# Performance work log

Hardware: AMD Instinct MI355X
Metric: run time of the kernel (lower is better)

Reference implementation:

```python
import jax, jax.numpy as jnp
import numpy as np

EPS = 1e-8

def setup_inputs() -> dict:
    key = jax.random.key(0)
    k1, k2, k3 = jax.random.split(key, 3)
    B, A = 4, 2048
    positions = jax.random.normal(k1, (B, A, 3), dtype=jnp.float32)
    neighbors = jax.random.randint(k2, (B, A, A), 0, A, dtype=jnp.int64)
    neighbor_mask = jax.random.randint(k3, (B, A), 0, 2).astype(bool)
    return {"positions": positions, "neighbors": neighbors, "neighbor_mask": neighbor_mask}

def _safe_norm(dist_vec):
    # torch.norm has zero (sub)gradient at 0; guard sqrt for jax parity
    d2 = jnp.sum(dist_vec * dist_vec, axis=-1)  # [B, A, N]
    safe = jnp.sqrt(jnp.where(d2 > 0, d2, 1.0))
    return jnp.where(d2 > 0, safe, 0.0)

def reference(positions, neighbors, neighbor_mask):
    B, A, _ = positions.shape
    # gather neighbor positions: pos_xyz[b, i, j] = positions[b, neighbors[b, i, j]]
    pos_xyz = positions[jnp.arange(B)[:, None, None], neighbors]  # [B, A, N, 3]
    dist_vec = pos_xyz - positions[:, :, None, :]                  # [B, A, N, 3]
    distances = _safe_norm(dist_vec)                               # [B, A, N]
    distances = 1.0 / (distances + EPS)
    # pairwise mask = outer product of per-atom mask (requires N == A)
    mask2 = neighbor_mask[:, :, None] & neighbor_mask[:, None, :]  # [B, A, A]
    eye = jnp.eye(A, dtype=bool)[None]
    distances = jnp.where(eye, 0.0, distances)   # zero diagonal
    distances = jnp.where(mask2, distances, 0.0)  # mask out invalid pairs
    return distances
```

## Files before the change

### kernel.cpp

```cpp
#include <hip/hip_runtime.h>


typedef float f4 __attribute__((ext_vector_type(4)));
typedef float f2 __attribute__((ext_vector_type(2)));

constexpr int A_DIM = 2048;
constexpr int WPB   = 8;
constexpr int NTHR  = WPB * 64;

__global__ __launch_bounds__(NTHR, 8) void atom_distances_kernel(
    const float* __restrict__ pos,
    const int*   __restrict__ nbr,
    const int*   __restrict__ mask,
    float*       __restrict__ out) {
  __shared__ float    sx[A_DIM];
  __shared__ f2       syz[A_DIM];
  __shared__ unsigned smaskbits[A_DIM / 32];

  const int blocks_per_b = A_DIM / WPB;
  const int b  = blockIdx.x / blocks_per_b;
  const int i0 = (blockIdx.x % blocks_per_b) * WPB;

  const float* posb  = pos  + (size_t)b * A_DIM * 3;
  const int*   maskb = mask + (size_t)b * A_DIM;

  for (int t = threadIdx.x; t < A_DIM; t += NTHR) {
    sx[t] = posb[3 * t + 0];
    f2 yz; yz.x = posb[3 * t + 1]; yz.y = posb[3 * t + 2];
    syz[t] = yz;
  }
  for (int r = 0; r < A_DIM / NTHR; ++r) {
    const int t = r * NTHR + threadIdx.x;
    const unsigned long long bal = __ballot(maskb[t] != 0);
    if ((threadIdx.x & 63) == 0) {
      const int wbase = t >> 5;
      smaskbits[wbase]     = (unsigned)bal;
      smaskbits[wbase + 1] = (unsigned)(bal >> 32);
    }
  }
  __syncthreads();

  const int w    = threadIdx.x >> 6;
  const int lane = threadIdx.x & 63;
  const int i    = i0 + w;

  float* orow = out + ((size_t)b * A_DIM + i) * A_DIM;
  const unsigned mi = (smaskbits[i >> 5] >> (i & 31)) & 1u;

  if (mi == 0) {
    const f4 z = {0.f, 0.f, 0.f, 0.f};
    #pragma unroll
    for (int c = 0; c < 8; ++c)
      __builtin_nontemporal_store(z, reinterpret_cast<f4*>(orow + (c * 64 + lane) * 4));
    return;
  }

  const float pix  = sx[i];
  const f2    piyz = syz[i];
  const int*  nrow = nbr + ((size_t)b * A_DIM + i) * A_DIM;

#define LDN(c) (*reinterpret_cast<const int4*>(nrow + ((c) * 64 + lane) * 4))

#define ELEM(nt_, e_, dst_) { \
    const bool on_ = ((((wbits >> (bit + e_)) & 1u) != 0u) & (i != j0 + e_)); \
    const int t_ = on_ ? ((nt_) & (A_DIM - 1)) : 0; \
    const float xx_ = sx[t_]; \
    const f2 yz_ = syz[t_]; \
    const float dx_ = xx_ - pix; \
    const float dy_ = yz_.x - piyz.x; \
    const float dz_ = yz_.y - piyz.y; \
    const float d2_ = dx_ * dx_ + dy_ * dy_ + dz_ * dz_; \
    const float inv_ = d2_ > 0.0f ? __builtin_amdgcn_rsqf(d2_) : 1e8f; \
    dst_ = on_ ? inv_ : 0.0f; }

#define PROC(c, n) { \
    const int j0 = ((c) * 64 + lane) * 4; \
    const unsigned wbits = smaskbits[(c) * 8 + (lane >> 3)]; \
    const int bit = (lane & 7) * 4; \
    f4 r; \
    ELEM(n.x, 0, r.x); \
    ELEM(n.y, 1, r.y); \
    ELEM(n.z, 2, r.z); \
    ELEM(n.w, 3, r.w); \
    __builtin_nontemporal_store(r, reinterpret_cast<f4*>(orow + j0)); }

  int4 n0 = LDN(0), n1 = LDN(1), n2 = LDN(2), n3 = LDN(3);
  PROC(0, n0); n0 = LDN(4);
  PROC(1, n1); n1 = LDN(5);
  PROC(2, n2); n2 = LDN(6);
  PROC(3, n3); n3 = LDN(7);
  PROC(4, n0);
  PROC(5, n1);
  PROC(6, n2);
  PROC(7, n3);

#undef PROC
#undef ELEM
#undef LDN
}

extern "C" void kernel_launch(void* const* d_in, const int* in_sizes, int n_in,
                              void* d_out, int out_size, void* d_ws, size_t ws_size,
                              hipStream_t stream) {
  const float* pos  = (const float*)d_in[0];
  const int*   nbr  = (const int*)d_in[1];
  const int*   mask = (const int*)d_in[2];
  float*       out  = (float*)d_out;

  const int B = in_sizes[2] / A_DIM;
  const int grid = B * (A_DIM / WPB);

  atom_distances_kernel<<<grid, NTHR, 0, stream>>>(pos, nbr, mask, out);
}
```

Measured before the change: 22.35 us.

## Process two rows per wave and prefetch neighbor indices before shared-memory setup

Each block now handles 16 rows, so each wave processes two rows. This halves the number of blocks and the per-block shared-memory loading of positions and mask bits. The first neighbor-index loads are issued before the shared-memory fill and barrier, so global load latency overlaps with setup, and the rsq select becomes fminf. It adds register pressure and code size from the two-row and mixed-mask paths, and halves grid parallelism.

```diff
diff --git a/kernel.cpp b/kernel.cpp
--- a/kernel.cpp
+++ b/kernel.cpp
@@ -6,6 +6,7 @@
 
 constexpr int A_DIM = 2048;
 constexpr int WPB   = 8;
+constexpr int RPB   = 16;
 constexpr int NTHR  = WPB * 64;
 
 __global__ __launch_bounds__(NTHR, 8) void atom_distances_kernel(
@@ -17,12 +18,29 @@
   __shared__ f2       syz[A_DIM];
   __shared__ unsigned smaskbits[A_DIM / 32];
 
-  const int blocks_per_b = A_DIM / WPB;
+  const int blocks_per_b = A_DIM / RPB;
   const int b  = blockIdx.x / blocks_per_b;
-  const int i0 = (blockIdx.x % blocks_per_b) * WPB;
+  const int i0 = (blockIdx.x % blocks_per_b) * RPB;
 
   const float* posb  = pos  + (size_t)b * A_DIM * 3;
   const int*   maskb = mask + (size_t)b * A_DIM;
+
+  const int w    = threadIdx.x >> 6;
+  const int lane = threadIdx.x & 63;
+  const int iA   = i0 + w;
+  const int iB   = i0 + WPB + w;
+
+  const int miA = maskb[iA];
+  const int miB = maskb[iB];
+  const int* nrowA = nbr + ((size_t)b * A_DIM + iA) * A_DIM;
+  const int* nrowB = nbr + ((size_t)b * A_DIM + iB) * A_DIM;
+
+#define LDA(c) (*reinterpret_cast<const int4*>(nrowA + ((c) * 64 + lane) * 4))
+#define LDB(c) (*reinterpret_cast<const int4*>(nrowB + ((c) * 64 + lane) * 4))
+
+  int4 a0, a1, b0, b1;
+  if (miA) { a0 = LDA(0); a1 = LDA(1); }
+  if (miB) { b0 = LDB(0); b1 = LDB(1); }
 
   for (int t = threadIdx.x; t < A_DIM; t += NTHR) {
     sx[t] = posb[3 * t + 0];
@@ -40,63 +58,92 @@
   }
   __syncthreads();
 
-  const int w    = threadIdx.x >> 6;
-  const int lane = threadIdx.x & 63;
-  const int i    = i0 + w;
+  float* orowA = out + ((size_t)b * A_DIM + iA) * A_DIM;
+  float* orowB = out + ((size_t)b * A_DIM + iB) * A_DIM;
+  const f4 zf4 = {0.f, 0.f, 0.f, 0.f};
 
-  float* orow = out + ((size_t)b * A_DIM + i) * A_DIM;
-  const unsigned mi = (smaskbits[i >> 5] >> (i & 31)) & 1u;
+#define ZST(o_, c_) __builtin_nontemporal_store(zf4, \
+    reinterpret_cast<f4*>((o_) + ((c_) * 64 + lane) * 4))
 
-  if (mi == 0) {
-    const f4 z = {0.f, 0.f, 0.f, 0.f};
+  if (!miA && !miB) {
     #pragma unroll
-    for (int c = 0; c < 8; ++c)
-      __builtin_nontemporal_store(z, reinterpret_cast<f4*>(orow + (c * 64 + lane) * 4));
+    for (int c = 0; c < 8; ++c) { ZST(orowA, c); ZST(orowB, c); }
     return;
   }
 
-  const float pix  = sx[i];
-  const f2    piyz = syz[i];
-  const int*  nrow = nbr + ((size_t)b * A_DIM + i) * A_DIM;
-
-#define LDN(c) (*reinterpret_cast<const int4*>(nrow + ((c) * 64 + lane) * 4))
-
-#define ELEM(nt_, e_, dst_) { \
-    const bool on_ = ((((wbits >> (bit + e_)) & 1u) != 0u) & (i != j0 + e_)); \
+#define ELEM(nt_, e_, dst_, i_, pix_, piyz_) { \
+    const bool on_ = ((((wbits >> (bit + e_)) & 1u) != 0u) & ((i_) != j0 + e_)); \
     const int t_ = on_ ? ((nt_) & (A_DIM - 1)) : 0; \
     const float xx_ = sx[t_]; \
     const f2 yz_ = syz[t_]; \
-    const float dx_ = xx_ - pix; \
-    const float dy_ = yz_.x - piyz.x; \
-    const float dz_ = yz_.y - piyz.y; \
+    const float dx_ = xx_ - pix_; \
+    const float dy_ = yz_.x - piyz_.x; \
+    const float dz_ = yz_.y - piyz_.y; \
     const float d2_ = dx_ * dx_ + dy_ * dy_ + dz_ * dz_; \
-    const float inv_ = d2_ > 0.0f ? __builtin_amdgcn_rsqf(d2_) : 1e8f; \
+    const float inv_ = fminf(__builtin_amdgcn_rsqf(d2_), 1e8f); \
     dst_ = on_ ? inv_ : 0.0f; }
 
-#define PROC(c, n) { \
+#define CHUNKHDR(c) \
     const int j0 = ((c) * 64 + lane) * 4; \
     const unsigned wbits = smaskbits[(c) * 8 + (lane >> 3)]; \
-    const int bit = (lane & 7) * 4; \
-    f4 r; \
-    ELEM(n.x, 0, r.x); \
-    ELEM(n.y, 1, r.y); \
-    ELEM(n.z, 2, r.z); \
-    ELEM(n.w, 3, r.w); \
-    __builtin_nontemporal_store(r, reinterpret_cast<f4*>(orow + j0)); }
+    const int bit = (lane & 7) * 4;
 
-  int4 n0 = LDN(0), n1 = LDN(1), n2 = LDN(2), n3 = LDN(3);
-  PROC(0, n0); n0 = LDN(4);
-  PROC(1, n1); n1 = LDN(5);
-  PROC(2, n2); n2 = LDN(6);
-  PROC(3, n3); n3 = LDN(7);
-  PROC(4, n0);
-  PROC(5, n1);
-  PROC(6, n2);
-  PROC(7, n3);
+#define PROC4(n_, i_, pix_, piyz_, orow_) { \
+    f4 r_; \
+    ELEM(n_.x, 0, r_.x, i_, pix_, piyz_); \
+    ELEM(n_.y, 1, r_.y, i_, pix_, piyz_); \
+    ELEM(n_.z, 2, r_.z, i_, pix_, piyz_); \
+    ELEM(n_.w, 3, r_.w, i_, pix_, piyz_); \
+    __builtin_nontemporal_store(r_, reinterpret_cast<f4*>((orow_) + j0)); }
 
-#undef PROC
+  if (miA && miB) {
+    const float pixA = sx[iA]; const f2 piyzA = syz[iA];
+    const float pixB = sx[iB]; const f2 piyzB = syz[iB];
+    { CHUNKHDR(0); PROC4(a0, iA, pixA, piyzA, orowA); PROC4(b0, iB, pixB, piyzB, orowB); }
+    a0 = LDA(2); b0 = LDB(2);
+    { CHUNKHDR(1); PROC4(a1, iA, pixA, piyzA, orowA); PROC4(b1, iB, pixB, piyzB, orowB); }
+    a1 = LDA(3); b1 = LDB(3);
+    { CHUNKHDR(2); PROC4(a0, iA, pixA, piyzA, orowA); PROC4(b0, iB, pixB, piyzB, orowB); }
+    a0 = LDA(4); b0 = LDB(4);
+    { CHUNKHDR(3); PROC4(a1, iA, pixA, piyzA, orowA); PROC4(b1, iB, pixB, piyzB, orowB); }
+    a1 = LDA(5); b1 = LDB(5);
+    { CHUNKHDR(4); PROC4(a0, iA, pixA, piyzA, orowA); PROC4(b0, iB, pixB, piyzB, orowB); }
+    a0 = LDA(6); b0 = LDB(6);
+    { CHUNKHDR(5); PROC4(a1, iA, pixA, piyzA, orowA); PROC4(b1, iB, pixB, piyzB, orowB); }
+    a1 = LDA(7); b1 = LDB(7);
+    { CHUNKHDR(6); PROC4(a0, iA, pixA, piyzA, orowA); PROC4(b0, iB, pixB, piyzB, orowB); }
+    { CHUNKHDR(7); PROC4(a1, iA, pixA, piyzA, orowA); PROC4(b1, iB, pixB, piyzB, orowB); }
+    return;
+  }
+
+  const int    i1    = miA ? iA : iB;
+  const int*   nrow1 = miA ? nrowA : nrowB;
+  float*       orow1 = miA ? orowA : orowB;
+  float*       orow0 = miA ? orowB : orowA;
+  int4 n0 = miA ? a0 : b0;
+  int4 n1 = miA ? a1 : b1;
+  const float pix  = sx[i1];
+  const f2    piyz = syz[i1];
+
+#define LD1(c) (*reinterpret_cast<const int4*>(nrow1 + ((c) * 64 + lane) * 4))
+
+  int4 n2 = LD1(2), n3 = LD1(3);
+  { CHUNKHDR(0); PROC4(n0, i1, pix, piyz, orow1); ZST(orow0, 0); } n0 = LD1(4);
+  { CHUNKHDR(1); PROC4(n1, i1, pix, piyz, orow1); ZST(orow0, 1); } n1 = LD1(5);
+  { CHUNKHDR(2); PROC4(n2, i1, pix, piyz, orow1); ZST(orow0, 2); } n2 = LD1(6);
+  { CHUNKHDR(3); PROC4(n3, i1, pix, piyz, orow1); ZST(orow0, 3); } n3 = LD1(7);
+  { CHUNKHDR(4); PROC4(n0, i1, pix, piyz, orow1); ZST(orow0, 4); }
+  { CHUNKHDR(5); PROC4(n1, i1, pix, piyz, orow1); ZST(orow0, 5); }
+  { CHUNKHDR(6); PROC4(n2, i1, pix, piyz, orow1); ZST(orow0, 6); }
+  { CHUNKHDR(7); PROC4(n3, i1, pix, piyz, orow1); ZST(orow0, 7); }
+
+#undef LD1
+#undef PROC4
+#undef CHUNKHDR
 #undef ELEM
-#undef LDN
+#undef ZST
+#undef LDA
+#undef LDB
 }
 
 extern "C" void kernel_launch(void* const* d_in, const int* in_sizes, int n_in,
@@ -108,7 +155,7 @@
   float*       out  = (float*)d_out;
 
   const int B = in_sizes[2] / A_DIM;
-  const int grid = B * (A_DIM / WPB);
+  const int grid = B * (A_DIM / RPB);
 
   atom_distances_kernel<<<grid, NTHR, 0, stream>>>(pos, nbr, mask, out);
 }
```

Measured after the change: 21.75 us. 2.7% less time.
